# Kernel optimization log

Hardware: AMD Instinct MI355X
Metric: run time of the kernel (lower is better)

The kernel has to match this reference:

```python
import jax, jax.numpy as jnp
import numpy as np

B, S, E, H, NQ, FF = 4, 1024, 256, 32, 8, 1024
DK = E // H  # 8, equals n_wires of the quantum attention layer
EPS = 1e-5


def layernorm(x, g, b):
    mu = jnp.mean(x, axis=-1, keepdims=True)
    var = jnp.mean(jnp.square(x - mu), axis=-1, keepdims=True)
    return (x - mu) * jax.lax.rsqrt(var + EPS) * g + b


def setup_inputs() -> dict:
    key = jax.random.key(0)
    ks = jax.random.split(key, 20)
    s = lambda n: 1.0 / np.sqrt(n)
    return {
        "x": jax.random.normal(ks[0], (B, S, E), dtype=jnp.float32),
        # quantum attention trainable RX angles (one per wire)
        "theta_attn": jax.random.uniform(ks[1], (DK,), minval=-np.pi, maxval=np.pi),
        # nn.MultiheadAttention packed in-proj and out-proj
        "w_in": jax.random.normal(ks[2], (3 * E, E)) * s(E),
        "b_in": jnp.zeros((3 * E,), jnp.float32),
        "w_out": jax.random.normal(ks[3], (E, E)) * s(E),
        "b_out": jnp.zeros((E,), jnp.float32),
        # combine linear
        "w_comb": jax.random.normal(ks[4], (E, E)) * s(E),
        "b_comb": jnp.zeros((E,), jnp.float32),
        # layernorms
        "g1": jnp.ones((E,), jnp.float32), "be1": jnp.zeros((E,), jnp.float32),
        "g2": jnp.ones((E,), jnp.float32), "be2": jnp.zeros((E,), jnp.float32),
        # FFN: input_proj, quantum RY angles, linear1, linear2
        "w_ip": jax.random.normal(ks[5], (NQ, E)) * s(E),
        "b_ip": jnp.zeros((NQ,), jnp.float32),
        "theta_ffn": jax.random.uniform(ks[6], (NQ,), minval=-np.pi, maxval=np.pi),
        "w1": jax.random.normal(ks[7], (FF, NQ)) * s(NQ),
        "b1": jnp.zeros((FF,), jnp.float32),
        "w2": jax.random.normal(ks[8], (E, FF)) * s(FF),
        "b2": jnp.zeros((E,), jnp.float32),
    }


def reference(x, theta_attn, w_in, b_in, w_out, b_out, w_comb, b_comb,
              g1, be1, g2, be2, w_ip, b_ip, theta_ffn, w1, b1, w2, b2):
    batch, seq, embed = x.shape
    # ---- QuantumAttention ----
    # per-head RX(x_i) encoding followed by trainable RX(theta_i): <Z_i> = cos(x_i + theta_i)
    xh = x.reshape(batch, seq, H, DK)            # [B,S,H,dk]
    q_out = jnp.cos(xh + theta_attn).reshape(batch, seq, embed)
    # standard multi-head self-attention on q_out (q=k=v)
    qkv = q_out @ w_in.T + b_in                  # [B,S,3E]
    q, k, v = jnp.split(qkv, 3, axis=-1)
    def heads(t):
        return t.reshape(batch, seq, H, DK).transpose(0, 2, 1, 3)  # [B,H,S,dk]
    q, k, v = heads(q), heads(k), heads(v)
    scores = jnp.einsum('bhqd,bhkd->bhqk', q, k) / np.sqrt(DK)
    attn = jax.nn.softmax(scores, axis=-1)
    ctx = jnp.einsum('bhqk,bhkd->bhqd', attn, v)
    ctx = ctx.transpose(0, 2, 1, 3).reshape(batch, seq, embed)
    attn_out = (ctx @ w_out.T + b_out) @ w_comb.T + b_comb
    # ---- residual + norm1 ----
    h = layernorm(x + attn_out, g1, be1)
    # ---- QuantumFeedForward ----
    proj = h @ w_ip.T + b_ip                     # [B,S,NQ]
    # RX(x) encoding then trainable RY(phi): <Z> = cos(phi) * cos(x)
    qf = jnp.cos(theta_ffn) * jnp.cos(proj)
    ffn_out = jax.nn.relu(qf @ w1.T + b1) @ w2.T + b2
    # ---- residual + norm2 ----
    return layernorm(h + ffn_out, g2, be2)
```

## Files before the change

kernel.cpp:

```cpp
#include <hip/hip_runtime.h>
#include <hip/hip_bf16.h>

#define B_  4
#define S_  1024
#define E_  256
#define H_  32
#define DK_ 8
#define NQ_ 8
#define FF_ 1024
#define M_  (B_*S_)
#define QS  0.5100880289202462f
#define VSTRIDE 1036

typedef __attribute__((ext_vector_type(8))) short bf16x8;
typedef __attribute__((ext_vector_type(4))) short short4v;
typedef __attribute__((ext_vector_type(4))) float f32x4;

__device__ inline short f2bf(float f) {
    union { float f; unsigned u; } v; v.f = f;
    unsigned r = (v.u + 0x7fff + ((v.u >> 16) & 1)) >> 16;
    return (short)r;
}

__device__ inline unsigned pk2(float a, float b) {
    __hip_bfloat162 h = __float22bfloat162_rn(make_float2(a, b));
    union { __hip_bfloat162 h; unsigned u; } c; c.h = h;
    return c.u;
}

__global__ __launch_bounds__(256) void prep_kernel(
        const float* __restrict__ x, const float* __restrict__ theta_attn,
        const float* __restrict__ w_in, const float* __restrict__ b_in,
        const float* __restrict__ w_out, const float* __restrict__ w_comb,
        const float* __restrict__ b_out, const float* __restrict__ b_comb,
        const float* __restrict__ w2,
        ushort* __restrict__ qout_bf, ushort* __restrict__ w_in_bf,
        float* __restrict__ b_in_s, ushort* __restrict__ w2_bf,
        ushort* __restrict__ w_comb_bf, ushort* __restrict__ w_outT_bf,
        float* __restrict__ zeros256, float* __restrict__ beff) {
    int blk = blockIdx.x, tid = threadIdx.x;
    __shared__ float red[4];
    if (blk < 512) {
        int i = blk * 256 + tid;
        float4 a = ((const float4*)x)[i * 2];
        float4 b = ((const float4*)x)[i * 2 + 1];
        bf16x8 o;
        o[0] = f2bf(__cosf(a.x + theta_attn[0]));
        o[1] = f2bf(__cosf(a.y + theta_attn[1]));
        o[2] = f2bf(__cosf(a.z + theta_attn[2]));
        o[3] = f2bf(__cosf(a.w + theta_attn[3]));
        o[4] = f2bf(__cosf(b.x + theta_attn[4]));
        o[5] = f2bf(__cosf(b.y + theta_attn[5]));
        o[6] = f2bf(__cosf(b.z + theta_attn[6]));
        o[7] = f2bf(__cosf(b.w + theta_attn[7]));
        *(bf16x8*)(qout_bf + (size_t)i * 8) = o;
    } else if (blk < 704) {
        int i = (blk - 512) * 256 + tid;
        float sc = (i < 16384) ? QS : 1.f;
        float4 v = ((const float4*)w_in)[i];
        short4v o = {f2bf(v.x * sc), f2bf(v.y * sc), f2bf(v.z * sc), f2bf(v.w * sc)};
        ((short4v*)w_in_bf)[i] = o;
    } else if (blk < 960) {
        int i = (blk - 704) * 256 + tid;
        float4 v = ((const float4*)w2)[i];
        short4v o = {f2bf(v.x), f2bf(v.y), f2bf(v.z), f2bf(v.w)};
        ((short4v*)w2_bf)[i] = o;
    } else if (blk < 1024) {
        int i = (blk - 960) * 256 + tid;
        float4 v = ((const float4*)w_comb)[i];
        short4v o = {f2bf(v.x), f2bf(v.y), f2bf(v.z), f2bf(v.w)};
        ((short4v*)w_comb_bf)[i] = o;
    } else if (blk < 1088) {
        int idx = (blk - 1024) * 256 + tid;
        int e = idx * 4, j = e >> 8, k0 = e & 255;
        short4v o;
#pragma unroll
        for (int i2 = 0; i2 < 4; ++i2) o[i2] = f2bf(w_out[(size_t)(k0 + i2) * 256 + j]);
        *(short4v*)(w_outT_bf + j * 256 + k0) = o;
    } else if (blk < 1089) {
        for (int r = 0; r < 3; ++r) {
            int i = r * 256 + tid;
            b_in_s[i] = b_in[i] * ((i < 256) ? QS : 1.f);
        }
        zeros256[tid] = 0.f;
    } else {
        int i = blk - 1089;
        float p = w_comb[(size_t)i * 256 + tid] * b_out[tid];
#pragma unroll
        for (int o = 32; o > 0; o >>= 1) p += __shfl_xor(p, o);
        if ((tid & 63) == 0) red[tid >> 6] = p;
        __syncthreads();
        if (tid == 0) beff[i] = red[0] + red[1] + red[2] + red[3] + b_comb[i];
    }
}

template<int OUT_BF16>
__global__ __launch_bounds__(256) void gemm_mfma_kernel(const ushort* __restrict__ A,
                                                        const ushort* __restrict__ W,
                                                        const float* __restrict__ bias,
                                                        void* __restrict__ Cv,
                                                        int Ndim, int Kdim) {
    __shared__ ushort As[128 * 64];
    __shared__ ushort Bs[64 * 64];
    int bm = blockIdx.y * 128, bn = blockIdx.x * 64;
    int tid = threadIdx.x;
    int w = tid >> 6, l = tid & 63, lq = l & 15, hi = l >> 4;
    int wm = w & 1, wn = w >> 1;
    f32x4 acc[4][2] = {};
    int srow = tid >> 3;
    int skb = (tid & 7) * 16;

    for (int k0 = 0; k0 < Kdim; k0 += 64) {
        __syncthreads();
#pragma unroll
        for (int it = 0; it < 4; ++it) {
            int row = it * 32 + srow;
            bf16x8 v = *(const bf16x8*)(A + (size_t)(bm + row) * Kdim + k0 + (skb >> 1));
            *(bf16x8*)((char*)As + row * 128 + (skb ^ ((row & 7) << 4))) = v;
        }
#pragma unroll
        for (int it = 0; it < 2; ++it) {
            int row = it * 32 + srow;
            bf16x8 v = *(const bf16x8*)(W + (size_t)(bn + row) * Kdim + k0 + (skb >> 1));
            *(bf16x8*)((char*)Bs + row * 128 + (skb ^ ((row & 7) << 4))) = v;
        }
        __syncthreads();
#pragma unroll
        for (int kk = 0; kk < 2; ++kk) {
            bf16x8 af[4], bfr[2];
#pragma unroll
            for (int mf = 0; mf < 4; ++mf) {
                int row = wm * 64 + mf * 16 + lq;
                af[mf] = *(const bf16x8*)((const char*)As + row * 128 +
                                          ((kk * 64 + hi * 16) ^ ((row & 7) << 4)));
            }
#pragma unroll
            for (int nf = 0; nf < 2; ++nf) {
                int row = wn * 32 + nf * 16 + lq;
                bfr[nf] = *(const bf16x8*)((const char*)Bs + row * 128 +
                                           ((kk * 64 + hi * 16) ^ ((row & 7) << 4)));
            }
#pragma unroll
            for (int mf = 0; mf < 4; ++mf)
#pragma unroll
                for (int nf = 0; nf < 2; ++nf)
                    acc[mf][nf] = __builtin_amdgcn_mfma_f32_16x16x32_bf16(af[mf], bfr[nf], acc[mf][nf], 0, 0, 0);
        }
    }
#pragma unroll
    for (int mf = 0; mf < 4; ++mf)
#pragma unroll
        for (int nf = 0; nf < 2; ++nf) {
            int n = bn + wn * 32 + nf * 16 + lq;
            float bv = bias[n];
#pragma unroll
            for (int r = 0; r < 4; ++r) {
                int m = bm + wm * 64 + mf * 16 + hi * 4 + r;
                float val = acc[mf][nf][r] + bv;
                if (OUT_BF16) ((ushort*)Cv)[(size_t)m * Ndim + n] = (ushort)f2bf(val);
                else ((float*)Cv)[(size_t)m * Ndim + n] = val;
            }
        }
}

__global__ __launch_bounds__(256, 4) void attn_mfma_kernel(const ushort* __restrict__ qkv,
                                                           ushort* __restrict__ ctx) {
    __shared__ ushort vt[9 * VSTRIDE + 4];
    int qt = blockIdx.x, h = blockIdx.y, b = blockIdx.z;
    int tid = threadIdx.x;
    const ushort* base = qkv + (size_t)b * S_ * (3 * E_) + h * 8;

    for (int i = tid; i < S_; i += 256) {
        bf16x8 vv = *(const bf16x8*)(base + (size_t)i * (3 * E_) + 2 * E_);
        int kf = (i >> 4) & 3, hh = (i >> 2) & 3, s = i & 3;
        int pv = (i & ~63) + ((kf >> 1) << 5) + (hh << 3) + ((kf & 1) << 2) + s;
#pragma unroll
        for (int d = 0; d < 8; ++d) vt[d * VSTRIDE + pv] = vv[d];
        vt[8 * VSTRIDE + pv] = 0x3F80;
    }
    __syncthreads();

    int w = tid >> 6, l = tid & 63, lq = l & 15, g = l >> 4;

    bf16x8 qfrag[2];
#pragma unroll
    for (int qf = 0; qf < 2; ++qf) {
        bf16x8 qv = {};
        if (g == 0)
            qv = *(const bf16x8*)(base + (size_t)(qt * 128 + w * 32 + qf * 16 + lq) * (3 * E_));
        qfrag[qf] = qv;
    }

    f32x4 ctxa[2] = {{0.f,0.f,0.f,0.f},{0.f,0.f,0.f,0.f}};

    for (int kt = 0; kt < 16; ++kt) {
        bf16x8 kfrag[4];
#pragma unroll
        for (int kf = 0; kf < 4; ++kf) {
            bf16x8 kv = {};
            if (g == 0)
                kv = *(const bf16x8*)(base + (size_t)(kt * 64 + kf * 16 + lq) * (3 * E_) + E_);
            kfrag[kf] = kv;
        }
        bf16x8 vf0 = *(bf16x8*)&vt[lq * VSTRIDE + kt * 64 + g * 8];
        bf16x8 vf1 = *(bf16x8*)&vt[lq * VSTRIDE + kt * 64 + 32 + g * 8];
#pragma unroll
        for (int qf = 0; qf < 2; ++qf) {
            f32x4 st[4];
#pragma unroll
            for (int kf = 0; kf < 4; ++kf) {
                f32x4 z = {0.f, 0.f, 0.f, 0.f};
                st[kf] = __builtin_amdgcn_mfma_f32_16x16x32_bf16(kfrag[kf], qfrag[qf], z, 0, 0, 0);
            }
            union { unsigned u[4]; bf16x8 v; } p0, p1;
            p0.u[0] = pk2(exp2f(st[0][0]), exp2f(st[0][1]));
            p0.u[1] = pk2(exp2f(st[0][2]), exp2f(st[0][3]));
            p0.u[2] = pk2(exp2f(st[1][0]), exp2f(st[1][1]));
            p0.u[3] = pk2(exp2f(st[1][2]), exp2f(st[1][3]));
            p1.u[0] = pk2(exp2f(st[2][0]), exp2f(st[2][1]));
            p1.u[1] = pk2(exp2f(st[2][2]), exp2f(st[2][3]));
            p1.u[2] = pk2(exp2f(st[3][0]), exp2f(st[3][1]));
            p1.u[3] = pk2(exp2f(st[3][2]), exp2f(st[3][3]));
            ctxa[qf] = __builtin_amdgcn_mfma_f32_16x16x32_bf16(p0.v, vf0, ctxa[qf], 0, 0, 0);
            ctxa[qf] = __builtin_amdgcn_mfma_f32_16x16x32_bf16(p1.v, vf1, ctxa[qf], 0, 0, 0);
        }
    }

#pragma unroll
    for (int qf = 0; qf < 2; ++qf) {
        int src = (l & 48) + 8;
        float s0 = __shfl(ctxa[qf][0], src);
        float s1 = __shfl(ctxa[qf][1], src);
        float s2 = __shfl(ctxa[qf][2], src);
        float s3 = __shfl(ctxa[qf][3], src);
        if (lq < 8) {
            int tok = b * S_ + qt * 128 + w * 32 + qf * 16 + g * 4;
            ushort* cp = ctx + (size_t)tok * E_ + h * 8 + lq;
            cp[0]       = (ushort)f2bf(ctxa[qf][0] / s0);
            cp[E_]      = (ushort)f2bf(ctxa[qf][1] / s1);
            cp[2 * E_]  = (ushort)f2bf(ctxa[qf][2] / s2);
            cp[3 * E_]  = (ushort)f2bf(ctxa[qf][3] / s3);
        }
    }
}

__global__ __launch_bounds__(256) void ln1_projqf_kernel(const float* __restrict__ a,
                                                         const float* __restrict__ r,
                                                         const float* __restrict__ g,
                                                         const float* __restrict__ be,
                                                         const float* __restrict__ w_ip,
                                                         const float* __restrict__ b_ip,
                                                         const float* __restrict__ theta,
                                                         float* __restrict__ h,
                                                         float* __restrict__ qf) {
    int wave = threadIdx.x >> 6, lane = threadIdx.x & 63;
    int token = blockIdx.x * 4 + wave;
    const float4 av = ((const float4*)(a + (size_t)token * E_))[lane];
    const float4 rv = ((const float4*)(r + (size_t)token * E_))[lane];
    float v0 = av.x + rv.x, v1 = av.y + rv.y, v2 = av.z + rv.z, v3 = av.w + rv.w;
    float sum = v0 + v1 + v2 + v3;
#pragma unroll
    for (int o = 32; o > 0; o >>= 1) sum += __shfl_xor(sum, o);
    float mu = sum * (1.f / E_);
    float d0 = v0 - mu, d1 = v1 - mu, d2 = v2 - mu, d3 = v3 - mu;
    float ss = d0 * d0 + d1 * d1 + d2 * d2 + d3 * d3;
#pragma unroll
    for (int o = 32; o > 0; o >>= 1) ss += __shfl_xor(ss, o);
    float rstd = rsqrtf(ss * (1.f / E_) + 1e-5f);
    float4 gv = ((const float4*)g)[lane];
    float4 bv = ((const float4*)be)[lane];
    float4 hv = make_float4(d0 * rstd * gv.x + bv.x, d1 * rstd * gv.y + bv.y,
                            d2 * rstd * gv.z + bv.z, d3 * rstd * gv.w + bv.w);
    ((float4*)(h + (size_t)token * E_))[lane] = hv;
    float acc[8];
#pragma unroll
    for (int w = 0; w < 8; ++w) {
        float4 wv = ((const float4*)(w_ip + w * E_))[lane];
        acc[w] = hv.x * wv.x + hv.y * wv.y + hv.z * wv.z + hv.w * wv.w;
    }
#pragma unroll
    for (int o = 32; o > 0; o >>= 1) {
#pragma unroll
        for (int w = 0; w < 8; ++w) acc[w] += __shfl_xor(acc[w], o);
    }
    if (lane == 0) {
#pragma unroll
        for (int w = 0; w < 8; ++w)
            qf[(size_t)token * NQ_ + w] = __cosf(theta[w]) * __cosf(acc[w] + b_ip[w]);
    }
}

__global__ __launch_bounds__(256) void resid_ln_kernel(const float* __restrict__ a,
                                                       const float* __restrict__ r,
                                                       const float* __restrict__ g,
                                                       const float* __restrict__ be,
                                                       float* __restrict__ out) {
    int wave = threadIdx.x >> 6, lane = threadIdx.x & 63;
    int token = blockIdx.x * 4 + wave;
    const float4 av = ((const float4*)(a + (size_t)token * E_))[lane];
    const float4 rv = ((const float4*)(r + (size_t)token * E_))[lane];
    float v0 = av.x + rv.x, v1 = av.y + rv.y, v2 = av.z + rv.z, v3 = av.w + rv.w;
    float sum = v0 + v1 + v2 + v3;
#pragma unroll
    for (int o = 32; o > 0; o >>= 1) sum += __shfl_xor(sum, o);
    float mu = sum * (1.f / E_);
    float d0 = v0 - mu, d1 = v1 - mu, d2 = v2 - mu, d3 = v3 - mu;
    float ss = d0 * d0 + d1 * d1 + d2 * d2 + d3 * d3;
#pragma unroll
    for (int o = 32; o > 0; o >>= 1) ss += __shfl_xor(ss, o);
    float rstd = rsqrtf(ss * (1.f / E_) + 1e-5f);
    float4 gv = ((const float4*)g)[lane];
    float4 bv = ((const float4*)be)[lane];
    float4 ov = make_float4(d0 * rstd * gv.x + bv.x, d1 * rstd * gv.y + bv.y,
                            d2 * rstd * gv.z + bv.z, d3 * rstd * gv.w + bv.w);
    ((float4*)(out + (size_t)token * E_))[lane] = ov;
}

__global__ __launch_bounds__(256) void ffn_t_kernel(const float* __restrict__ qf,
                                                    const float* __restrict__ w1,
                                                    const float* __restrict__ b1,
                                                    ushort* __restrict__ t) {
    int idx = blockIdx.x * 256 + threadIdx.x;
    int token = idx >> 7;
    int fb = (idx & 127) * 8;
    const float* qp = qf + (size_t)token * NQ_;
    float4 q0 = ((const float4*)qp)[0], q1 = ((const float4*)qp)[1];
    bf16x8 o;
#pragma unroll
    for (int j = 0; j < 8; ++j) {
        const float* wp = w1 + (size_t)(fb + j) * NQ_;
        float4 w0 = ((const float4*)wp)[0], w1v = ((const float4*)wp)[1];
        float s = b1[fb + j] + q0.x * w0.x + q0.y * w0.y + q0.z * w0.z + q0.w * w0.w
                + q1.x * w1v.x + q1.y * w1v.y + q1.z * w1v.z + q1.w * w1v.w;
        o[j] = f2bf(fmaxf(s, 0.f));
    }
    *(bf16x8*)(t + (size_t)idx * 8) = o;
}

extern "C" void kernel_launch(void* const* d_in, const int* in_sizes, int n_in,
                              void* d_out, int out_size, void* d_ws, size_t ws_size,
                              hipStream_t stream) {
    const float* x          = (const float*)d_in[0];
    const float* theta_attn = (const float*)d_in[1];
    const float* w_in       = (const float*)d_in[2];
    const float* b_in       = (const float*)d_in[3];
    const float* w_out      = (const float*)d_in[4];
    const float* b_out      = (const float*)d_in[5];
    const float* w_comb     = (const float*)d_in[6];
    const float* b_comb     = (const float*)d_in[7];
    const float* g1         = (const float*)d_in[8];
    const float* be1        = (const float*)d_in[9];
    const float* g2         = (const float*)d_in[10];
    const float* be2        = (const float*)d_in[11];
    const float* w_ip       = (const float*)d_in[12];
    const float* b_ip       = (const float*)d_in[13];
    const float* theta_ffn  = (const float*)d_in[14];
    const float* w1         = (const float*)d_in[15];
    const float* b1         = (const float*)d_in[16];
    const float* w2         = (const float*)d_in[17];
    const float* b2         = (const float*)d_in[18];
    float* out = (float*)d_out;

    char* wsb = (char*)d_ws;
    ushort* qout_bf  = (ushort*)(wsb + 0);
    ushort* qkv_bf   = (ushort*)(wsb + (2u << 20));
    ushort* t_bf     = (ushort*)(wsb + 0);
    ushort* ctx_bf   = (ushort*)(wsb + (8u << 20));
    ushort* w_comb_bf= (ushort*)(wsb + (8u << 20));
    ushort* w_outT_bf= (ushort*)(wsb + (8u << 20) + 131072);
    float*  attn_out = (float*)(wsb + (10u << 20));
    float*  ffn_out  = attn_out;
    float*  h        = (float*)(wsb + (14u << 20));
    ushort* w_in_bf  = (ushort*)(wsb + (18u << 20));
    ushort* w2_bf    = (ushort*)(wsb + (18u << 20) + 393216);
    ushort* weff_bf  = (ushort*)(wsb + (18u << 20) + 917504);
    float*  beff     = (float*)(wsb + (18u << 20) + 1048576);
    float*  zeros256 = (float*)(wsb + (18u << 20) + 1052672);
    float*  b_in_s   = (float*)(wsb + (18u << 20) + 1056768);
    float*  qf       = (float*)(wsb + (18u << 20) + 1060864);

    prep_kernel<<<1345, 256, 0, stream>>>(x, theta_attn, w_in, b_in, w_out, w_comb,
                                          b_out, b_comb, w2,
                                          qout_bf, w_in_bf, b_in_s, w2_bf,
                                          w_comb_bf, w_outT_bf, zeros256, beff);
    gemm_mfma_kernel<1><<<dim3(4, 2), 256, 0, stream>>>(w_comb_bf, w_outT_bf, zeros256, weff_bf, E_, E_);
    gemm_mfma_kernel<1><<<dim3(768 / 64, M_ / 128), 256, 0, stream>>>(qout_bf, w_in_bf, b_in_s, qkv_bf, 768, E_);
    attn_mfma_kernel<<<dim3(S_ / 128, H_, B_), 256, 0, stream>>>(qkv_bf, ctx_bf);
    gemm_mfma_kernel<0><<<dim3(E_ / 64, M_ / 128), 256, 0, stream>>>(ctx_bf, weff_bf, beff, attn_out, E_, E_);
    ln1_projqf_kernel<<<M_ / 4, 256, 0, stream>>>(x, attn_out, g1, be1, w_ip, b_ip, theta_ffn, h, qf);
    ffn_t_kernel<<<(M_ * FF_) / (256 * 8), 256, 0, stream>>>(qf, w1, b1, t_bf);
    gemm_mfma_kernel<0><<<dim3(E_ / 64, M_ / 128), 256, 0, stream>>>(t_bf, w2_bf, b2, ffn_out, E_, FF_);
    resid_ln_kernel<<<M_ / 4, 256, 0, stream>>>(h, ffn_out, g2, be2, out);
}
```

Measured before the change: 204.9 us.

## Fuse pipeline into four kernels with in-GEMM prep and LayerNorm epilogues

Replaces the nine-launch pipeline with four kernels. The first computes the cosine encoding and weight conversion directly inside the QKV and weight-combine GEMM tiles, alongside bias folding and w2 conversion. The out-projection GEMM is fused with residual, LayerNorm1, the FFN input projection and the first FFN layer, and the second FFN GEMM is fused with residual and LayerNorm2. This removes launch overhead and intermediate fp32 round trips. In exchange it adds redundant weight conversion per tile, uses one-pass variance, and switches to a hardware exp2 builtin.

```diff
diff --git a/kernel.cpp b/kernel.cpp
--- a/kernel.cpp
+++ b/kernel.cpp
@@ -5,7 +5,6 @@
 #define S_  1024
 #define E_  256
 #define H_  32
-#define DK_ 8
 #define NQ_ 8
 #define FF_ 1024
 #define M_  (B_*S_)
@@ -16,113 +15,128 @@
 typedef __attribute__((ext_vector_type(4))) short short4v;
 typedef __attribute__((ext_vector_type(4))) float f32x4;
 
+#if __has_builtin(__builtin_amdgcn_exp2f)
+#define EXP2 __builtin_amdgcn_exp2f
+#else
+#define EXP2 exp2f
+#endif
+
 __device__ inline short f2bf(float f) {
     union { float f; unsigned u; } v; v.f = f;
     unsigned r = (v.u + 0x7fff + ((v.u >> 16) & 1)) >> 16;
     return (short)r;
 }
 
+__device__ inline float bf2f(ushort u_) {
+    union { unsigned u; float f; } c; c.u = ((unsigned)u_) << 16; return c.f;
+}
+
 __device__ inline unsigned pk2(float a, float b) {
     __hip_bfloat162 h = __float22bfloat162_rn(make_float2(a, b));
     union { __hip_bfloat162 h; unsigned u; } c; c.h = h;
     return c.u;
 }
 
-__global__ __launch_bounds__(256) void prep_kernel(
+__global__ __launch_bounds__(256) void d1_kernel(
         const float* __restrict__ x, const float* __restrict__ theta_attn,
         const float* __restrict__ w_in, const float* __restrict__ b_in,
         const float* __restrict__ w_out, const float* __restrict__ w_comb,
         const float* __restrict__ b_out, const float* __restrict__ b_comb,
         const float* __restrict__ w2,
-        ushort* __restrict__ qout_bf, ushort* __restrict__ w_in_bf,
-        float* __restrict__ b_in_s, ushort* __restrict__ w2_bf,
-        ushort* __restrict__ w_comb_bf, ushort* __restrict__ w_outT_bf,
-        float* __restrict__ zeros256, float* __restrict__ beff) {
-    int blk = blockIdx.x, tid = threadIdx.x;
-    __shared__ float red[4];
-    if (blk < 512) {
-        int i = blk * 256 + tid;
-        float4 a = ((const float4*)x)[i * 2];
-        float4 b = ((const float4*)x)[i * 2 + 1];
-        bf16x8 o;
-        o[0] = f2bf(__cosf(a.x + theta_attn[0]));
-        o[1] = f2bf(__cosf(a.y + theta_attn[1]));
-        o[2] = f2bf(__cosf(a.z + theta_attn[2]));
-        o[3] = f2bf(__cosf(a.w + theta_attn[3]));
-        o[4] = f2bf(__cosf(b.x + theta_attn[4]));
-        o[5] = f2bf(__cosf(b.y + theta_attn[5]));
-        o[6] = f2bf(__cosf(b.z + theta_attn[6]));
-        o[7] = f2bf(__cosf(b.w + theta_attn[7]));
-        *(bf16x8*)(qout_bf + (size_t)i * 8) = o;
-    } else if (blk < 704) {
-        int i = (blk - 512) * 256 + tid;
-        float sc = (i < 16384) ? QS : 1.f;
-        float4 v = ((const float4*)w_in)[i];
-        short4v o = {f2bf(v.x * sc), f2bf(v.y * sc), f2bf(v.z * sc), f2bf(v.w * sc)};
-        ((short4v*)w_in_bf)[i] = o;
-    } else if (blk < 960) {
-        int i = (blk - 704) * 256 + tid;
-        float4 v = ((const float4*)w2)[i];
-        short4v o = {f2bf(v.x), f2bf(v.y), f2bf(v.z), f2bf(v.w)};
-        ((short4v*)w2_bf)[i] = o;
-    } else if (blk < 1024) {
-        int i = (blk - 960) * 256 + tid;
-        float4 v = ((const float4*)w_comb)[i];
-        short4v o = {f2bf(v.x), f2bf(v.y), f2bf(v.z), f2bf(v.w)};
-        ((short4v*)w_comb_bf)[i] = o;
-    } else if (blk < 1088) {
-        int idx = (blk - 1024) * 256 + tid;
-        int e = idx * 4, j = e >> 8, k0 = e & 255;
-        short4v o;
-#pragma unroll
-        for (int i2 = 0; i2 < 4; ++i2) o[i2] = f2bf(w_out[(size_t)(k0 + i2) * 256 + j]);
-        *(short4v*)(w_outT_bf + j * 256 + k0) = o;
-    } else if (blk < 1089) {
-        for (int r = 0; r < 3; ++r) {
-            int i = r * 256 + tid;
-            b_in_s[i] = b_in[i] * ((i < 256) ? QS : 1.f);
-        }
-        zeros256[tid] = 0.f;
-    } else {
-        int i = blk - 1089;
-        float p = w_comb[(size_t)i * 256 + tid] * b_out[tid];
-#pragma unroll
-        for (int o = 32; o > 0; o >>= 1) p += __shfl_xor(p, o);
-        if ((tid & 63) == 0) red[tid >> 6] = p;
-        __syncthreads();
-        if (tid == 0) beff[i] = red[0] + red[1] + red[2] + red[3] + b_comb[i];
-    }
-}
-
-template<int OUT_BF16>
-__global__ __launch_bounds__(256) void gemm_mfma_kernel(const ushort* __restrict__ A,
-                                                        const ushort* __restrict__ W,
-                                                        const float* __restrict__ bias,
-                                                        void* __restrict__ Cv,
-                                                        int Ndim, int Kdim) {
+        ushort* __restrict__ qkv_bf, ushort* __restrict__ weff_bf,
+        float* __restrict__ beff, ushort* __restrict__ w2_bf) {
     __shared__ ushort As[128 * 64];
     __shared__ ushort Bs[64 * 64];
-    int bm = blockIdx.y * 128, bn = blockIdx.x * 64;
-    int tid = threadIdx.x;
+    __shared__ float red[4];
+    int bid = blockIdx.x, tid = threadIdx.x;
+
+    if (bid >= 392) {
+        if (bid < 648) {
+            int i = bid - 392;
+            float p = w_comb[(size_t)i * 256 + tid] * b_out[tid];
+#pragma unroll
+            for (int o = 32; o > 0; o >>= 1) p += __shfl_xor(p, o);
+            if ((tid & 63) == 0) red[tid >> 6] = p;
+            __syncthreads();
+            if (tid == 0) beff[i] = red[0] + red[1] + red[2] + red[3] + b_comb[i];
+        } else {
+            int i = (bid - 648) * 256 + tid;
+            float4 v = ((const float4*)w2)[i];
+            short4v o = {f2bf(v.x), f2bf(v.y), f2bf(v.z), f2bf(v.w)};
+            ((short4v*)w2_bf)[i] = o;
+        }
+        return;
+    }
+
+    bool isW = bid >= 384;
+    int bm, bn;
+    if (!isW) { bm = (bid / 12) * 128; bn = (bid % 12) * 64; }
+    else      { int t = bid - 384; bm = (t >> 2) * 128; bn = (t & 3) * 64; }
+
     int w = tid >> 6, l = tid & 63, lq = l & 15, hi = l >> 4;
     int wm = w & 1, wn = w >> 1;
     f32x4 acc[4][2] = {};
     int srow = tid >> 3;
-    int skb = (tid & 7) * 16;
-
-    for (int k0 = 0; k0 < Kdim; k0 += 64) {
+    int sk = (tid & 7) * 8;
+    float wscale = isW ? 1.f : ((bn < 256) ? QS : 1.f);
+    float th[8];
+    if (!isW) {
+#pragma unroll
+        for (int j = 0; j < 8; ++j) th[j] = theta_attn[j];
+    }
+
+    for (int k0 = 0; k0 < 256; k0 += 64) {
         __syncthreads();
-#pragma unroll
-        for (int it = 0; it < 4; ++it) {
-            int row = it * 32 + srow;
-            bf16x8 v = *(const bf16x8*)(A + (size_t)(bm + row) * Kdim + k0 + (skb >> 1));
-            *(bf16x8*)((char*)As + row * 128 + (skb ^ ((row & 7) << 4))) = v;
-        }
-#pragma unroll
-        for (int it = 0; it < 2; ++it) {
-            int row = it * 32 + srow;
-            bf16x8 v = *(const bf16x8*)(W + (size_t)(bn + row) * Kdim + k0 + (skb >> 1));
-            *(bf16x8*)((char*)Bs + row * 128 + (skb ^ ((row & 7) << 4))) = v;
+        if (!isW) {
+#pragma unroll
+            for (int it = 0; it < 4; ++it) {
+                int row = it * 32 + srow;
+                const float* xp = x + (size_t)(bm + row) * 256 + k0 + sk;
+                float4 a = *(const float4*)xp;
+                float4 b = *(const float4*)(xp + 4);
+                bf16x8 o;
+                o[0] = f2bf(__cosf(a.x + th[0]));
+                o[1] = f2bf(__cosf(a.y + th[1]));
+                o[2] = f2bf(__cosf(a.z + th[2]));
+                o[3] = f2bf(__cosf(a.w + th[3]));
+                o[4] = f2bf(__cosf(b.x + th[4]));
+                o[5] = f2bf(__cosf(b.y + th[5]));
+                o[6] = f2bf(__cosf(b.z + th[6]));
+                o[7] = f2bf(__cosf(b.w + th[7]));
+                *(bf16x8*)((char*)As + row * 128 + ((sk * 2) ^ ((row & 7) << 4))) = o;
+            }
+#pragma unroll
+            for (int it = 0; it < 2; ++it) {
+                int row = it * 32 + srow;
+                const float* wp = w_in + (size_t)(bn + row) * 256 + k0 + sk;
+                float4 a = *(const float4*)wp;
+                float4 b = *(const float4*)(wp + 4);
+                bf16x8 o;
+                o[0] = f2bf(a.x * wscale); o[1] = f2bf(a.y * wscale);
+                o[2] = f2bf(a.z * wscale); o[3] = f2bf(a.w * wscale);
+                o[4] = f2bf(b.x * wscale); o[5] = f2bf(b.y * wscale);
+                o[6] = f2bf(b.z * wscale); o[7] = f2bf(b.w * wscale);
+                *(bf16x8*)((char*)Bs + row * 128 + ((sk * 2) ^ ((row & 7) << 4))) = o;
+            }
+        } else {
+#pragma unroll
+            for (int it = 0; it < 4; ++it) {
+                int row = it * 32 + srow;
+                const float* wp = w_comb + (size_t)(bm + row) * 256 + k0 + sk;
+                float4 a = *(const float4*)wp;
+                float4 b = *(const float4*)(wp + 4);
+                bf16x8 o;
+                o[0] = f2bf(a.x); o[1] = f2bf(a.y); o[2] = f2bf(a.z); o[3] = f2bf(a.w);
+                o[4] = f2bf(b.x); o[5] = f2bf(b.y); o[6] = f2bf(b.z); o[7] = f2bf(b.w);
+                *(bf16x8*)((char*)As + row * 128 + ((sk * 2) ^ ((row & 7) << 4))) = o;
+            }
+            int nl = tid & 63, kg = tid >> 6;
+#pragma unroll
+            for (int kk = 0; kk < 16; ++kk) {
+                int kb = (kg * 16 + kk) * 2;
+                float v = w_out[(size_t)(k0 + kg * 16 + kk) * 256 + bn + nl];
+                *(ushort*)((char*)Bs + nl * 128 + (kb ^ ((nl & 7) << 4))) = (ushort)f2bf(v);
+            }
         }
         __syncthreads();
 #pragma unroll
@@ -147,18 +161,18 @@
                     acc[mf][nf] = __builtin_amdgcn_mfma_f32_16x16x32_bf16(af[mf], bfr[nf], acc[mf][nf], 0, 0, 0);
         }
     }
+    ushort* Cp = isW ? weff_bf : qkv_bf;
+    int Nd = isW ? 256 : 768;
 #pragma unroll
     for (int mf = 0; mf < 4; ++mf)
 #pragma unroll
         for (int nf = 0; nf < 2; ++nf) {
             int n = bn + wn * 32 + nf * 16 + lq;
-            float bv = bias[n];
+            float bv = isW ? 0.f : b_in[n] * wscale;
 #pragma unroll
             for (int r = 0; r < 4; ++r) {
                 int m = bm + wm * 64 + mf * 16 + hi * 4 + r;
-                float val = acc[mf][nf][r] + bv;
-                if (OUT_BF16) ((ushort*)Cv)[(size_t)m * Ndim + n] = (ushort)f2bf(val);
-                else ((float*)Cv)[(size_t)m * Ndim + n] = val;
+                Cp[(size_t)m * Nd + n] = (ushort)f2bf(acc[mf][nf][r] + bv);
             }
         }
 }
@@ -192,6 +206,7 @@
     }
 
     f32x4 ctxa[2] = {{0.f,0.f,0.f,0.f},{0.f,0.f,0.f,0.f}};
+    const f32x4 zf = {0.f, 0.f, 0.f, 0.f};
 
     for (int kt = 0; kt < 16; ++kt) {
         bf16x8 kfrag[4];
@@ -208,19 +223,17 @@
         for (int qf = 0; qf < 2; ++qf) {
             f32x4 st[4];
 #pragma unroll
-            for (int kf = 0; kf < 4; ++kf) {
-                f32x4 z = {0.f, 0.f, 0.f, 0.f};
-                st[kf] = __builtin_amdgcn_mfma_f32_16x16x32_bf16(kfrag[kf], qfrag[qf], z, 0, 0, 0);
-            }
+            for (int kf = 0; kf < 4; ++kf)
+                st[kf] = __builtin_amdgcn_mfma_f32_16x16x32_bf16(kfrag[kf], qfrag[qf], zf, 0, 0, 0);
             union { unsigned u[4]; bf16x8 v; } p0, p1;
-            p0.u[0] = pk2(exp2f(st[0][0]), exp2f(st[0][1]));
-            p0.u[1] = pk2(exp2f(st[0][2]), exp2f(st[0][3]));
-            p0.u[2] = pk2(exp2f(st[1][0]), exp2f(st[1][1]));
-            p0.u[3] = pk2(exp2f(st[1][2]), exp2f(st[1][3]));
-            p1.u[0] = pk2(exp2f(st[2][0]), exp2f(st[2][1]));
-            p1.u[1] = pk2(exp2f(st[2][2]), exp2f(st[2][3]));
-            p1.u[2] = pk2(exp2f(st[3][0]), exp2f(st[3][1]));
-            p1.u[3] = pk2(exp2f(st[3][2]), exp2f(st[3][3]));
+            p0.u[0] = pk2(EXP2(st[0][0]), EXP2(st[0][1]));
+            p0.u[1] = pk2(EXP2(st[0][2]), EXP2(st[0][3]));
+            p0.u[2] = pk2(EXP2(st[1][0]), EXP2(st[1][1]));
+            p0.u[3] = pk2(EXP2(st[1][2]), EXP2(st[1][3]));
+            p1.u[0] = pk2(EXP2(st[2][0]), EXP2(st[2][1]));
+            p1.u[1] = pk2(EXP2(st[2][2]), EXP2(st[2][3]));
+            p1.u[2] = pk2(EXP2(st[3][0]), EXP2(st[3][1]));
+            p1.u[3] = pk2(EXP2(st[3][2]), EXP2(st[3][3]));
             ctxa[qf] = __builtin_amdgcn_mfma_f32_16x16x32_bf16(p0.v, vf0, ctxa[qf], 0, 0, 0);
             ctxa[qf] = __builtin_amdgcn_mfma_f32_16x16x32_bf16(p1.v, vf1, ctxa[qf], 0, 0, 0);
         }
@@ -236,105 +249,296 @@
         if (lq < 8) {
             int tok = b * S_ + qt * 128 + w * 32 + qf * 16 + g * 4;
             ushort* cp = ctx + (size_t)tok * E_ + h * 8 + lq;
-            cp[0]       = (ushort)f2bf(ctxa[qf][0] / s0);
-            cp[E_]      = (ushort)f2bf(ctxa[qf][1] / s1);
-            cp[2 * E_]  = (ushort)f2bf(ctxa[qf][2] / s2);
-            cp[3 * E_]  = (ushort)f2bf(ctxa[qf][3] / s3);
-        }
-    }
-}
-
-__global__ __launch_bounds__(256) void ln1_projqf_kernel(const float* __restrict__ a,
-                                                         const float* __restrict__ r,
-                                                         const float* __restrict__ g,
-                                                         const float* __restrict__ be,
-                                                         const float* __restrict__ w_ip,
-                                                         const float* __restrict__ b_ip,
-                                                         const float* __restrict__ theta,
-                                                         float* __restrict__ h,
-                                                         float* __restrict__ qf) {
-    int wave = threadIdx.x >> 6, lane = threadIdx.x & 63;
-    int token = blockIdx.x * 4 + wave;
-    const float4 av = ((const float4*)(a + (size_t)token * E_))[lane];
-    const float4 rv = ((const float4*)(r + (size_t)token * E_))[lane];
-    float v0 = av.x + rv.x, v1 = av.y + rv.y, v2 = av.z + rv.z, v3 = av.w + rv.w;
-    float sum = v0 + v1 + v2 + v3;
-#pragma unroll
-    for (int o = 32; o > 0; o >>= 1) sum += __shfl_xor(sum, o);
-    float mu = sum * (1.f / E_);
-    float d0 = v0 - mu, d1 = v1 - mu, d2 = v2 - mu, d3 = v3 - mu;
-    float ss = d0 * d0 + d1 * d1 + d2 * d2 + d3 * d3;
-#pragma unroll
-    for (int o = 32; o > 0; o >>= 1) ss += __shfl_xor(ss, o);
-    float rstd = rsqrtf(ss * (1.f / E_) + 1e-5f);
-    float4 gv = ((const float4*)g)[lane];
-    float4 bv = ((const float4*)be)[lane];
-    float4 hv = make_float4(d0 * rstd * gv.x + bv.x, d1 * rstd * gv.y + bv.y,
-                            d2 * rstd * gv.z + bv.z, d3 * rstd * gv.w + bv.w);
-    ((float4*)(h + (size_t)token * E_))[lane] = hv;
-    float acc[8];
-#pragma unroll
-    for (int w = 0; w < 8; ++w) {
-        float4 wv = ((const float4*)(w_ip + w * E_))[lane];
-        acc[w] = hv.x * wv.x + hv.y * wv.y + hv.z * wv.z + hv.w * wv.w;
-    }
-#pragma unroll
-    for (int o = 32; o > 0; o >>= 1) {
-#pragma unroll
-        for (int w = 0; w < 8; ++w) acc[w] += __shfl_xor(acc[w], o);
-    }
-    if (lane == 0) {
-#pragma unroll
-        for (int w = 0; w < 8; ++w)
-            qf[(size_t)token * NQ_ + w] = __cosf(theta[w]) * __cosf(acc[w] + b_ip[w]);
-    }
-}
-
-__global__ __launch_bounds__(256) void resid_ln_kernel(const float* __restrict__ a,
-                                                       const float* __restrict__ r,
-                                                       const float* __restrict__ g,
-                                                       const float* __restrict__ be,
-                                                       float* __restrict__ out) {
-    int wave = threadIdx.x >> 6, lane = threadIdx.x & 63;
-    int token = blockIdx.x * 4 + wave;
-    const float4 av = ((const float4*)(a + (size_t)token * E_))[lane];
-    const float4 rv = ((const float4*)(r + (size_t)token * E_))[lane];
-    float v0 = av.x + rv.x, v1 = av.y + rv.y, v2 = av.z + rv.z, v3 = av.w + rv.w;
-    float sum = v0 + v1 + v2 + v3;
-#pragma unroll
-    for (int o = 32; o > 0; o >>= 1) sum += __shfl_xor(sum, o);
-    float mu = sum * (1.f / E_);
-    float d0 = v0 - mu, d1 = v1 - mu, d2 = v2 - mu, d3 = v3 - mu;
-    float ss = d0 * d0 + d1 * d1 + d2 * d2 + d3 * d3;
-#pragma unroll
-    for (int o = 32; o > 0; o >>= 1) ss += __shfl_xor(ss, o);
-    float rstd = rsqrtf(ss * (1.f / E_) + 1e-5f);
-    float4 gv = ((const float4*)g)[lane];
-    float4 bv = ((const float4*)be)[lane];
-    float4 ov = make_float4(d0 * rstd * gv.x + bv.x, d1 * rstd * gv.y + bv.y,
-                            d2 * rstd * gv.z + bv.z, d3 * rstd * gv.w + bv.w);
-    ((float4*)(out + (size_t)token * E_))[lane] = ov;
-}
-
-__global__ __launch_bounds__(256) void ffn_t_kernel(const float* __restrict__ qf,
-                                                    const float* __restrict__ w1,
-                                                    const float* __restrict__ b1,
-                                                    ushort* __restrict__ t) {
-    int idx = blockIdx.x * 256 + threadIdx.x;
-    int token = idx >> 7;
-    int fb = (idx & 127) * 8;
-    const float* qp = qf + (size_t)token * NQ_;
-    float4 q0 = ((const float4*)qp)[0], q1 = ((const float4*)qp)[1];
-    bf16x8 o;
-#pragma unroll
-    for (int j = 0; j < 8; ++j) {
-        const float* wp = w1 + (size_t)(fb + j) * NQ_;
-        float4 w0 = ((const float4*)wp)[0], w1v = ((const float4*)wp)[1];
-        float s = b1[fb + j] + q0.x * w0.x + q0.y * w0.y + q0.z * w0.z + q0.w * w0.w
-                + q1.x * w1v.x + q1.y * w1v.y + q1.z * w1v.z + q1.w * w1v.w;
-        o[j] = f2bf(fmaxf(s, 0.f));
-    }
-    *(bf16x8*)(t + (size_t)idx * 8) = o;
+            cp[0]      = (ushort)f2bf(ctxa[qf][0] / s0);
+            cp[E_]     = (ushort)f2bf(ctxa[qf][1] / s1);
+            cp[2 * E_] = (ushort)f2bf(ctxa[qf][2] / s2);
+            cp[3 * E_] = (ushort)f2bf(ctxa[qf][3] / s3);
+        }
+    }
+}
+
+__global__ __launch_bounds__(512) void d3_kernel(
+        const ushort* __restrict__ ctx, const ushort* __restrict__ weff,
+        const float* __restrict__ beff, const float* __restrict__ x,
+        const float* __restrict__ g1, const float* __restrict__ be1,
+        const float* __restrict__ w_ip, const float* __restrict__ b_ip,
+        const float* __restrict__ theta_ffn,
+        const float* __restrict__ w1, const float* __restrict__ b1,
+        float* __restrict__ h, ushort* __restrict__ t_bf) {
+    __shared__ union {
+        struct { ushort As[64 * 64]; ushort Bs[256 * 64]; } st;
+        struct { ushort hl[64 * 264]; float qfl[64 * 9]; ushort w1l[8192]; } ph;
+    } u;
+    __shared__ float red[2][64][4];
+    int tid = threadIdx.x;
+    int bm = blockIdx.x * 64;
+    int w = tid >> 6, l = tid & 63, lq = l & 15, hi = l >> 4;
+    int wm = w >> 2, wn = w & 3;
+    f32x4 acc[2][4] = {};
+    int srow = tid >> 3, sk = (tid & 7) * 8;
+
+    for (int k0 = 0; k0 < 256; k0 += 64) {
+        __syncthreads();
+        {
+            bf16x8 v = *(const bf16x8*)(ctx + (size_t)(bm + srow) * 256 + k0 + sk);
+            *(bf16x8*)((char*)u.st.As + srow * 128 + ((sk * 2) ^ ((srow & 7) << 4))) = v;
+        }
+#pragma unroll
+        for (int it = 0; it < 4; ++it) {
+            int v8 = it * 512 + tid;
+            int row = v8 >> 3, kb = (v8 & 7) * 16;
+            bf16x8 v = *(const bf16x8*)(weff + (size_t)row * 256 + k0 + (kb >> 1));
+            *(bf16x8*)((char*)u.st.Bs + row * 128 + (kb ^ ((row & 7) << 4))) = v;
+        }
+        __syncthreads();
+#pragma unroll
+        for (int kk = 0; kk < 2; ++kk) {
+            bf16x8 af[2], bfr[4];
+#pragma unroll
+            for (int mf = 0; mf < 2; ++mf) {
+                int row = wm * 32 + mf * 16 + lq;
+                af[mf] = *(const bf16x8*)((const char*)u.st.As + row * 128 +
+                                          ((kk * 64 + hi * 16) ^ ((row & 7) << 4)));
+            }
+#pragma unroll
+            for (int nf = 0; nf < 4; ++nf) {
+                int row = wn * 64 + nf * 16 + lq;
+                bfr[nf] = *(const bf16x8*)((const char*)u.st.Bs + row * 128 +
+                                           ((kk * 64 + hi * 16) ^ ((row & 7) << 4)));
+            }
+#pragma unroll
+            for (int mf = 0; mf < 2; ++mf)
+#pragma unroll
+                for (int nf = 0; nf < 4; ++nf)
+                    acc[mf][nf] = __builtin_amdgcn_mfma_f32_16x16x32_bf16(af[mf], bfr[nf], acc[mf][nf], 0, 0, 0);
+        }
+    }
+    __syncthreads();
+
+    float bv[4];
+#pragma unroll
+    for (int nf = 0; nf < 4; ++nf) bv[nf] = beff[wn * 64 + nf * 16 + lq];
+    float vv[2][4][4];
+    float rs[2][4] = {}, rq[2][4] = {};
+#pragma unroll
+    for (int mf = 0; mf < 2; ++mf)
+#pragma unroll
+        for (int nf = 0; nf < 4; ++nf) {
+            int n = wn * 64 + nf * 16 + lq;
+#pragma unroll
+            for (int r = 0; r < 4; ++r) {
+                int m = bm + wm * 32 + mf * 16 + hi * 4 + r;
+                float val = acc[mf][nf][r] + bv[nf] + x[(size_t)m * 256 + n];
+                vv[mf][nf][r] = val;
+                rs[mf][r] += val;
+                rq[mf][r] += val * val;
+            }
+        }
+#pragma unroll
+    for (int o = 1; o < 16; o <<= 1)
+#pragma unroll
+        for (int mf = 0; mf < 2; ++mf)
+#pragma unroll
+            for (int r = 0; r < 4; ++r) {
+                rs[mf][r] += __shfl_xor(rs[mf][r], o);
+                rq[mf][r] += __shfl_xor(rq[mf][r], o);
+            }
+    if (lq == 0) {
+#pragma unroll
+        for (int mf = 0; mf < 2; ++mf)
+#pragma unroll
+            for (int r = 0; r < 4; ++r) {
+                int row = wm * 32 + mf * 16 + hi * 4 + r;
+                red[0][row][wn] = rs[mf][r];
+                red[1][row][wn] = rq[mf][r];
+            }
+    }
+    __syncthreads();
+#pragma unroll
+    for (int mf = 0; mf < 2; ++mf)
+#pragma unroll
+        for (int r = 0; r < 4; ++r) {
+            int row = wm * 32 + mf * 16 + hi * 4 + r;
+            float st_ = red[0][row][0] + red[0][row][1] + red[0][row][2] + red[0][row][3];
+            float sq_ = red[1][row][0] + red[1][row][1] + red[1][row][2] + red[1][row][3];
+            float mu = st_ * (1.f / 256.f);
+            float var = sq_ * (1.f / 256.f) - mu * mu;
+            rs[mf][r] = mu;
+            rq[mf][r] = rsqrtf(var + 1e-5f);
+        }
+#pragma unroll
+    for (int mf = 0; mf < 2; ++mf)
+#pragma unroll
+        for (int nf = 0; nf < 4; ++nf) {
+            int n = wn * 64 + nf * 16 + lq;
+            float gn = g1[n], bn_ = be1[n];
+#pragma unroll
+            for (int r = 0; r < 4; ++r) {
+                int row = wm * 32 + mf * 16 + hi * 4 + r;
+                float vn = (vv[mf][nf][r] - rs[mf][r]) * rq[mf][r] * gn + bn_;
+                h[(size_t)(bm + row) * 256 + n] = vn;
+                u.ph.hl[row * 264 + n] = (ushort)f2bf(vn);
+            }
+        }
+    for (int i = tid; i < 8192; i += 512) u.ph.w1l[i] = (ushort)f2bf(w1[i]);
+    __syncthreads();
+
+    {
+        int tok = tid >> 3, wq = tid & 7;
+        const float* wip = w_ip + wq * 256;
+        float pr = 0.f;
+#pragma unroll
+        for (int c = 0; c < 32; ++c) {
+            bf16x8 hv = *(const bf16x8*)&u.ph.hl[tok * 264 + c * 8];
+            float4 wa = *(const float4*)(wip + c * 8);
+            float4 wb = *(const float4*)(wip + c * 8 + 4);
+            pr += bf2f((ushort)hv[0]) * wa.x + bf2f((ushort)hv[1]) * wa.y
+                + bf2f((ushort)hv[2]) * wa.z + bf2f((ushort)hv[3]) * wa.w
+                + bf2f((ushort)hv[4]) * wb.x + bf2f((ushort)hv[5]) * wb.y
+                + bf2f((ushort)hv[6]) * wb.z + bf2f((ushort)hv[7]) * wb.w;
+        }
+        u.ph.qfl[tok * 9 + wq] = __cosf(theta_ffn[wq]) * __cosf(pr + b_ip[wq]);
+    }
+    __syncthreads();
+
+    for (int it = 0; it < 16; ++it) {
+        int idx = it * 512 + tid;
+        int tok = idx >> 7, fb = (idx & 127) * 8;
+        float q[8];
+#pragma unroll
+        for (int j = 0; j < 8; ++j) q[j] = u.ph.qfl[tok * 9 + j];
+        float4 ba = *(const float4*)(b1 + fb);
+        float4 bb = *(const float4*)(b1 + fb + 4);
+        float sa[8] = {ba.x, ba.y, ba.z, ba.w, bb.x, bb.y, bb.z, bb.w};
+        bf16x8 o;
+#pragma unroll
+        for (int j = 0; j < 8; ++j) {
+            bf16x8 wv = *(const bf16x8*)&u.ph.w1l[(fb + j) * 8];
+            float s = sa[j];
+#pragma unroll
+            for (int k = 0; k < 8; ++k) s += q[k] * bf2f((ushort)wv[k]);
+            o[j] = f2bf(fmaxf(s, 0.f));
+        }
+        *(bf16x8*)(t_bf + (size_t)(bm + tok) * 1024 + fb) = o;
+    }
+}
+
+__global__ __launch_bounds__(512) void d4_kernel(
+        const ushort* __restrict__ t_bf, const ushort* __restrict__ w2b,
+        const float* __restrict__ b2, const float* __restrict__ h,
+        const float* __restrict__ g2, const float* __restrict__ be2,
+        float* __restrict__ out) {
+    __shared__ ushort As[64 * 64];
+    __shared__ ushort Bs[256 * 64];
+    __shared__ float red[2][64][4];
+    int tid = threadIdx.x;
+    int bm = blockIdx.x * 64;
+    int w = tid >> 6, l = tid & 63, lq = l & 15, hi = l >> 4;
+    int wm = w >> 2, wn = w & 3;
+    f32x4 acc[2][4] = {};
+    int srow = tid >> 3, sk = (tid & 7) * 8;
+
+    for (int k0 = 0; k0 < 1024; k0 += 64) {
+        __syncthreads();
+        {
+            bf16x8 v = *(const bf16x8*)(t_bf + (size_t)(bm + srow) * 1024 + k0 + sk);
+            *(bf16x8*)((char*)As + srow * 128 + ((sk * 2) ^ ((srow & 7) << 4))) = v;
+        }
+#pragma unroll
+        for (int it = 0; it < 4; ++it) {
+            int v8 = it * 512 + tid;
+            int row = v8 >> 3, kb = (v8 & 7) * 16;
+            bf16x8 v = *(const bf16x8*)(w2b + (size_t)row * 1024 + k0 + (kb >> 1));
+            *(bf16x8*)((char*)Bs + row * 128 + (kb ^ ((row & 7) << 4))) = v;
+        }
+        __syncthreads();
+#pragma unroll
+        for (int kk = 0; kk < 2; ++kk) {
+            bf16x8 af[2], bfr[4];
+#pragma unroll
+            for (int mf = 0; mf < 2; ++mf) {
+                int row = wm * 32 + mf * 16 + lq;
+                af[mf] = *(const bf16x8*)((const char*)As + row * 128 +
+                                          ((kk * 64 + hi * 16) ^ ((row & 7) << 4)));
+            }
+#pragma unroll
+            for (int nf = 0; nf < 4; ++nf) {
+                int row = wn * 64 + nf * 16 + lq;
+                bfr[nf] = *(const bf16x8*)((const char*)Bs + row * 128 +
+                                           ((kk * 64 + hi * 16) ^ ((row & 7) << 4)));
+            }
+#pragma unroll
+            for (int mf = 0; mf < 2; ++mf)
+#pragma unroll
+                for (int nf = 0; nf < 4; ++nf)
+                    acc[mf][nf] = __builtin_amdgcn_mfma_f32_16x16x32_bf16(af[mf], bfr[nf], acc[mf][nf], 0, 0, 0);
+        }
+    }
+
+    float bv[4];
+#pragma unroll
+    for (int nf = 0; nf < 4; ++nf) bv[nf] = b2[wn * 64 + nf * 16 + lq];
+    float vv[2][4][4];
+    float rs[2][4] = {}, rq[2][4] = {};
+#pragma unroll
+    for (int mf = 0; mf < 2; ++mf)
+#pragma unroll
+        for (int nf = 0; nf < 4; ++nf) {
+            int n = wn * 64 + nf * 16 + lq;
+#pragma unroll
+            for (int r = 0; r < 4; ++r) {
+                int m = bm + wm * 32 + mf * 16 + hi * 4 + r;
+                float val = acc[mf][nf][r] + bv[nf] + h[(size_t)m * 256 + n];
+                vv[mf][nf][r] = val;
+                rs[mf][r] += val;
+                rq[mf][r] += val * val;
+            }
+        }
+#pragma unroll
+    for (int o = 1; o < 16; o <<= 1)
+#pragma unroll
+        for (int mf = 0; mf < 2; ++mf)
+#pragma unroll
+            for (int r = 0; r < 4; ++r) {
+                rs[mf][r] += __shfl_xor(rs[mf][r], o);
+                rq[mf][r] += __shfl_xor(rq[mf][r], o);
+            }
+    if (lq == 0) {
+#pragma unroll
+        for (int mf = 0; mf < 2; ++mf)
+#pragma unroll
+            for (int r = 0; r < 4; ++r) {
+                int row = wm * 32 + mf * 16 + hi * 4 + r;
+                red[0][row][wn] = rs[mf][r];
+                red[1][row][wn] = rq[mf][r];
+            }
+    }
+    __syncthreads();
+#pragma unroll
+    for (int mf = 0; mf < 2; ++mf)
+#pragma unroll
+        for (int r = 0; r < 4; ++r) {
+            int row = wm * 32 + mf * 16 + hi * 4 + r;
+            float st_ = red[0][row][0] + red[0][row][1] + red[0][row][2] + red[0][row][3];
+            float sq_ = red[1][row][0] + red[1][row][1] + red[1][row][2] + red[1][row][3];
+            float mu = st_ * (1.f / 256.f);
+            float var = sq_ * (1.f / 256.f) - mu * mu;
+            rs[mf][r] = mu;
+            rq[mf][r] = rsqrtf(var + 1e-5f);
+        }
+#pragma unroll
+    for (int mf = 0; mf < 2; ++mf)
+#pragma unroll
+        for (int nf = 0; nf < 4; ++nf) {
+            int n = wn * 64 + nf * 16 + lq;
+            float gn = g2[n], bn_ = be2[n];
+#pragma unroll
+            for (int r = 0; r < 4; ++r) {
+                int row = wm * 32 + mf * 16 + hi * 4 + r;
+                out[(size_t)(bm + row) * 256 + n] =
+                    (vv[mf][nf][r] - rs[mf][r]) * rq[mf][r] * gn + bn_;
+            }
+        }
 }
 
 extern "C" void kernel_launch(void* const* d_in, const int* in_sizes, int n_in,
@@ -362,33 +566,18 @@
     float* out = (float*)d_out;
 
     char* wsb = (char*)d_ws;
-    ushort* qout_bf  = (ushort*)(wsb + 0);
-    ushort* qkv_bf   = (ushort*)(wsb + (2u << 20));
-    ushort* t_bf     = (ushort*)(wsb + 0);
-    ushort* ctx_bf   = (ushort*)(wsb + (8u << 20));
-    ushort* w_comb_bf= (ushort*)(wsb + (8u << 20));
-    ushort* w_outT_bf= (ushort*)(wsb + (8u << 20) + 131072);
-    float*  attn_out = (float*)(wsb + (10u << 20));
-    float*  ffn_out  = attn_out;
-    float*  h        = (float*)(wsb + (14u << 20));
-    ushort* w_in_bf  = (ushort*)(wsb + (18u << 20));
-    ushort* w2_bf    = (ushort*)(wsb + (18u << 20) + 393216);
-    ushort* weff_bf  = (ushort*)(wsb + (18u << 20) + 917504);
-    float*  beff     = (float*)(wsb + (18u << 20) + 1048576);
-    float*  zeros256 = (float*)(wsb + (18u << 20) + 1052672);
-    float*  b_in_s   = (float*)(wsb + (18u << 20) + 1056768);
-    float*  qf       = (float*)(wsb + (18u << 20) + 1060864);
-
-    prep_kernel<<<1345, 256, 0, stream>>>(x, theta_attn, w_in, b_in, w_out, w_comb,
-                                          b_out, b_comb, w2,
-                                          qout_bf, w_in_bf, b_in_s, w2_bf,
-                                          w_comb_bf, w_outT_bf, zeros256, beff);
-    gemm_mfma_kernel<1><<<dim3(4, 2), 256, 0, stream>>>(w_comb_bf, w_outT_bf, zeros256, weff_bf, E_, E_);
-    gemm_mfma_kernel<1><<<dim3(768 / 64, M_ / 128), 256, 0, stream>>>(qout_bf, w_in_bf, b_in_s, qkv_bf, 768, E_);
+    ushort* qkv_bf  = (ushort*)(wsb);
+    ushort* ctx_bf  = (ushort*)(wsb + (6u << 20));
+    ushort* t_bf    = (ushort*)(wsb + (8u << 20));
+    float*  h       = (float*)(wsb + (16u << 20));
+    ushort* weff_bf = (ushort*)(wsb + (20u << 20));
+    ushort* w2_bf   = (ushort*)(wsb + (20u << 20) + 131072);
+    float*  beff    = (float*)(wsb + (20u << 20) + 655360);
+
+    d1_kernel<<<904, 256, 0, stream>>>(x, theta_attn, w_in, b_in, w_out, w_comb,
+                                       b_out, b_comb, w2, qkv_bf, weff_bf, beff, w2_bf);
     attn_mfma_kernel<<<dim3(S_ / 128, H_, B_), 256, 0, stream>>>(qkv_bf, ctx_bf);
-    gemm_mfma_kernel<0><<<dim3(E_ / 64, M_ / 128), 256, 0, stream>>>(ctx_bf, weff_bf, beff, attn_out, E_, E_);
-    ln1_projqf_kernel<<<M_ / 4, 256, 0, stream>>>(x, attn_out, g1, be1, w_ip, b_ip, theta_ffn, h, qf);
-    ffn_t_kernel<<<(M_ * FF_) / (256 * 8), 256, 0, stream>>>(qf, w1, b1, t_bf);
-    gemm_mfma_kernel<0><<<dim3(E_ / 64, M_ / 128), 256, 0, stream>>>(t_bf, w2_bf, b2, ffn_out, E_, FF_);
-    resid_ln_kernel<<<M_ / 4, 256, 0, stream>>>(h, ffn_out, g2, be2, out);
-}
+    d3_kernel<<<M_ / 64, 512, 0, stream>>>(ctx_bf, weff_bf, beff, x, g1, be1,
+                                           w_ip, b_ip, theta_ffn, w1, b1, h, t_bf);
+    d4_kernel<<<M_ / 64, 512, 0, stream>>>(t_bf, w2_bf, b2, h, g2, be2, out);
+}
```

Result: slower. 217.4 us (+6.1%).
